# Kernel tuning notes

Measured on AMD Instinct MI355X. Metric: run time of the kernel, lower is better.

Reference implementation:

```python
import jax, jax.numpy as jnp
import numpy as np
import math

B, C, H, W = 4, 256, 64, 64
E = 96  # embed_dim
SOFTMAX_SCALE = 10.0
RESIDUAL_SCALE_INIT = 0.1


def conv1x1(w, x):
    # w: [out_c, in_c], x: [b, in_c, h, w] -> [b, out_c, h, w]
    return jnp.einsum('oc,bchw->bohw', w, x)


def setup_inputs() -> dict:
    key = jax.random.key(0)
    ks = jax.random.split(key, 12)
    s = 0.02
    return {
        'x': jax.random.normal(ks[0], (B, C, H, W), jnp.float32),
        'mask': jax.random.uniform(ks[1], (B, 1, H, W), jnp.float32),
        'ln_gamma': jnp.ones((C,), jnp.float32),
        'ln_beta': jnp.zeros((C,), jnp.float32),
        'wq': jax.random.normal(ks[2], (E, C), jnp.float32) * s,
        'wk': jax.random.normal(ks[3], (E, C), jnp.float32) * s,
        'wv': jax.random.normal(ks[4], (C, C), jnp.float32) * s,
        'w_out': jax.random.normal(ks[5], (C, C), jnp.float32) * s,
        'w_qm': jax.random.normal(ks[6], (E, 1), jnp.float32) * s,
        'wd1': jax.random.normal(ks[7], (C, 2 * C), jnp.float32) * s,
        'wd2': jax.random.normal(ks[8], (C, C), jnp.float32) * s,
        'wg': jax.random.normal(ks[9], (C, C + 1), jnp.float32) * s,
        'residual_scale': jnp.asarray(RESIDUAL_SCALE_INIT, jnp.float32),
    }


def reference(x, mask, ln_gamma, ln_beta, wq, wk, wv, w_out, w_qm, wd1, wd2, wg,
              residual_scale):
    b, c, h, w = x.shape
    n = h * w

    # ChannelLayerNorm: LayerNorm over channel dim
    mu = jnp.mean(x, axis=1, keepdims=True)
    var = jnp.mean((x - mu) ** 2, axis=1, keepdims=True)
    x_norm = (x - mu) / jnp.sqrt(var + 1e-5)
    x_norm = x_norm * ln_gamma[None, :, None, None] + ln_beta[None, :, None, None]

    # Q/K/V projections (1x1 convs), flatten to [b, n, d]
    q = conv1x1(wq, x_norm) + conv1x1(w_qm, mask)
    q = q.reshape(b, E, n).transpose(0, 2, 1)        # [b, n, E]
    k = conv1x1(wk, x_norm).reshape(b, E, n).transpose(0, 2, 1)  # [b, n, E]
    v = conv1x1(wv, x).reshape(b, c, n).transpose(0, 2, 1)       # [b, n, C]

    # cosine normalization (F.normalize with eps=1e-12)
    q = q / jnp.clip(jnp.linalg.norm(q, axis=-1, keepdims=True), 1e-12)
    k = k / jnp.clip(jnp.linalg.norm(k, axis=-1, keepdims=True), 1e-12)

    scale = SOFTMAX_SCALE / math.sqrt(E)
    attn = jnp.einsum('bqe,bke->bqk', q, k) * scale  # [b, n, n]

    # keys with mask >= 0.5 are invalid -> bias -10000
    invalid_keys = (mask.reshape(b, 1, n) >= 0.5)    # [b, 1, n]
    attn = jnp.where(invalid_keys, jnp.float32(-10000.0), attn)
    attn = jax.nn.softmax(attn, axis=-1)

    attended = jnp.einsum('bqk,bkc->bqc', attn, v)   # [b, n, C]
    attended = attended.transpose(0, 2, 1).reshape(b, c, h, w)
    attended = conv1x1(w_out, attended)

    # delta correction branch
    corr_in = jnp.concatenate([attended - x, x_norm * mask], axis=1)  # [b, 2C, h, w]
    hidden = jax.nn.gelu(conv1x1(wd1, corr_in), approximate=False)
    corrective = conv1x1(wd2, hidden)

    # MaskConditionedGate (assumed): sigmoid(1x1 conv over [corrective, mask])
    gate_in = jnp.concatenate([corrective, mask], axis=1)  # [b, C+1, h, w]
    gate = jax.nn.sigmoid(conv1x1(wg, gate_in)) * mask

    delta = jnp.tanh(residual_scale) * gate * corrective
    return x + delta
```

## Files before the change

### kernel.cpp

```cpp
#include <hip/hip_runtime.h>
#include <hip/hip_bf16.h>
#include <math.h>

#define BB 4
#define CC 256
#define NN 4096
#define EE 96
#define NTOT (BB*NN)

typedef __attribute__((ext_vector_type(8))) short bf16x8;
typedef __attribute__((ext_vector_type(4))) float f32x4;

__device__ __forceinline__ short f2bf(float x) {
    __hip_bfloat16 h = __float2bfloat16(x);
    return *reinterpret_cast<short*>(&h);
}
__device__ __forceinline__ float bf2f(short s) {
    unsigned int u = ((unsigned int)(unsigned short)s) << 16;
    float f;
    __builtin_memcpy(&f, &u, 4);
    return f;
}
__device__ __forceinline__ float gelu_exact(float v) {
    return 0.5f * v * (1.0f + erff(v * 0.70710678118654752f));
}
__device__ __forceinline__ void gld16(void* lds, const void* g) {
    __builtin_amdgcn_global_load_lds(
        (const __attribute__((address_space(1))) unsigned int*)g,
        (__attribute__((address_space(3))) unsigned int*)lds, 16, 0, 0);
}

#define OFF_WQ  0
#define OFF_WK  24576
#define OFF_WV  49152
#define OFF_WO  114688
#define OFF_WD1 180224
#define OFF_WD2 311296
#define OFF_WG  376832
#define OFF_WGL 442368
#define W16_TOTAL 442624

__global__ void wconv_kernel(const float* __restrict__ wq, const float* __restrict__ wk,
                             const float* __restrict__ wv, const float* __restrict__ wo,
                             const float* __restrict__ wd1, const float* __restrict__ wd2,
                             const float* __restrict__ wg, short* __restrict__ W16) {
    int i = blockIdx.x * 256 + threadIdx.x;
    if (i >= W16_TOTAL) return;
    float v;
    if      (i < OFF_WK)  v = wq[i];
    else if (i < OFF_WV)  v = wk[i - OFF_WK];
    else if (i < OFF_WO)  v = wv[i - OFF_WV];
    else if (i < OFF_WD1) v = wo[i - OFF_WO];
    else if (i < OFF_WD2) v = wd1[i - OFF_WD1];
    else if (i < OFF_WG)  v = wd2[i - OFF_WD2];
    else if (i < OFF_WGL) { int l = i - OFF_WG; v = wg[(l >> 8) * 257 + (l & 255)]; }
    else                  v = wg[(i - OFF_WGL) * 257 + 256];
    W16[i] = f2bf(v);
}

__global__ __launch_bounds__(256) void ln_kernel(
    const float* __restrict__ x, const float* __restrict__ gamma,
    const float* __restrict__ beta,
    short* __restrict__ Xt16, short* __restrict__ Xn16) {
    __shared__ float tile[256 * 33];
    __shared__ float psum[8][32], psq[8][32];
    __shared__ float mu_s[32], rs_s[32];
    __shared__ float gs[256], bs[256];
    const int b  = blockIdx.x >> 7;
    const int p0 = (blockIdx.x & 127) * 32;
    const int tid = threadIdx.x;
    const float* xb = x + (size_t)b * CC * NN;

    gs[tid] = gamma[tid];
    bs[tid] = beta[tid];
    #pragma unroll
    for (int i = 0; i < 8; ++i) {
        int idx = tid + i * 256;
        int c = idx >> 3, p4 = (idx & 7) * 4;
        float4 v = *(const float4*)&xb[(size_t)c * NN + p0 + p4];
        tile[c * 33 + p4]     = v.x;
        tile[c * 33 + p4 + 1] = v.y;
        tile[c * 33 + p4 + 2] = v.z;
        tile[c * 33 + p4 + 3] = v.w;
    }
    __syncthreads();
    {
        int col = tid & 31, part = tid >> 5;
        float s = 0.f, sq = 0.f;
        for (int r = part * 32; r < part * 32 + 32; ++r) {
            float v = tile[r * 33 + col];
            s += v; sq += v * v;
        }
        psum[part][col] = s; psq[part][col] = sq;
    }
    __syncthreads();
    if (tid < 32) {
        float S = 0.f, SQ = 0.f;
        #pragma unroll
        for (int j = 0; j < 8; ++j) { S += psum[j][tid]; SQ += psq[j][tid]; }
        float mu = S / 256.0f;
        float var = SQ / 256.0f - mu * mu;
        mu_s[tid] = mu;
        rs_s[tid] = rsqrtf(var + 1e-5f);
    }
    __syncthreads();
    size_t rowbase = ((size_t)b * NN + p0) * CC;
    #pragma unroll
    for (int i = 0; i < 4; ++i) {
        int idx = tid + i * 256;
        int p = idx >> 5, c8 = (idx & 31) * 8;
        float mu = mu_s[p], rcp = rs_s[p];
        bf16x8 xt, xn;
        #pragma unroll
        for (int j = 0; j < 8; ++j) {
            float v = tile[(c8 + j) * 33 + p];
            float n = (v - mu) * rcp * gs[c8 + j] + bs[c8 + j];
            xt[j] = f2bf(v); xn[j] = f2bf(n);
        }
        size_t o = rowbase + (size_t)p * CC + c8;
        *(bf16x8*)&Xt16[o] = xt;
        *(bf16x8*)&Xn16[o] = xn;
    }
}

__global__ __launch_bounds__(256) void qkproj_kernel(
    const short* __restrict__ Xn16, const short* __restrict__ W16,
    const float* __restrict__ mask, const float* __restrict__ w_qm,
    short* __restrict__ Q16, short* __restrict__ K16)
{
    const int tid = threadIdx.x;
    const int w = tid >> 6, lane = tid & 63, ln = lane & 15, quad = lane >> 4;
    const int m0 = blockIdx.x * 32 + (w & 1) * 16;
    const bool isQ = (w < 2);
    const int woff = isQ ? OFF_WQ : OFF_WK;

    f32x4 acc[6];
    #pragma unroll
    for (int i = 0; i < 6; ++i) acc[i] = (f32x4){0.f, 0.f, 0.f, 0.f};

    #pragma unroll
    for (int kt = 0; kt < 8; ++kt) {
        bf16x8 af = *(const bf16x8*)&Xn16[(size_t)(m0 + ln) * 256 + kt * 32 + quad * 8];
        #pragma unroll
        for (int nt = 0; nt < 6; ++nt) {
            bf16x8 bf = *(const bf16x8*)&W16[woff + (size_t)(nt * 16 + ln) * 256 + kt * 32 + quad * 8];
            acc[nt] = __builtin_amdgcn_mfma_f32_16x16x32_bf16(af, bf, acc[nt], 0, 0, 0);
        }
    }

    short* outp = isQ ? Q16 : K16;
    #pragma unroll
    for (int r = 0; r < 4; ++r) {
        int row = m0 + quad * 4 + r;
        float mrow = isQ ? mask[row] : 0.f;
        float vals[6];
        float ss = 0.f;
        #pragma unroll
        for (int nt = 0; nt < 6; ++nt) {
            float v = acc[nt][r];
            if (isQ) v += mrow * w_qm[nt * 16 + ln];
            vals[nt] = v;
            ss += v * v;
        }
        ss += __shfl_xor(ss, 1, 64); ss += __shfl_xor(ss, 2, 64);
        ss += __shfl_xor(ss, 4, 64); ss += __shfl_xor(ss, 8, 64);
        float sc = 1.0f / fmaxf(sqrtf(ss), 1e-12f);
        #pragma unroll
        for (int nt = 0; nt < 6; ++nt)
            outp[(size_t)row * EE + nt * 16 + ln] = f2bf(vals[nt] * sc);
    }
}

__global__ __launch_bounds__(256) void vproj_kernel(
    const short* __restrict__ Xt16, const short* __restrict__ W16,
    short* __restrict__ V16t)
{
    __shared__ short Vt[256 * 40];
    const int tid = threadIdx.x;
    const int w = tid >> 6, lane = tid & 63, ln = lane & 15, quad = lane >> 4;
    const int m0 = blockIdx.x * 32;
    const int wm = w >> 1, wn = w & 1;
    const int mrow = m0 + wm * 16;

    f32x4 acc[8];
    #pragma unroll
    for (int i = 0; i < 8; ++i) acc[i] = (f32x4){0.f, 0.f, 0.f, 0.f};

    #pragma unroll
    for (int kt = 0; kt < 8; ++kt) {
        bf16x8 af = *(const bf16x8*)&Xt16[(size_t)(mrow + ln) * 256 + kt * 32 + quad * 8];
        #pragma unroll
        for (int nt = 0; nt < 8; ++nt) {
            int col = wn * 128 + nt * 16 + ln;
            bf16x8 bf = *(const bf16x8*)&W16[OFF_WV + (size_t)col * 256 + kt * 32 + quad * 8];
            acc[nt] = __builtin_amdgcn_mfma_f32_16x16x32_bf16(af, bf, acc[nt], 0, 0, 0);
        }
    }
    #pragma unroll
    for (int nt = 0; nt < 8; ++nt) {
        int ch = wn * 128 + nt * 16 + ln;
        #pragma unroll
        for (int r = 0; r < 4; ++r)
            Vt[ch * 40 + wm * 16 + quad * 4 + r] = f2bf(acc[nt][r]);
    }
    __syncthreads();
    const int b = m0 >> 12, p0l = m0 & 4095;
    #pragma unroll
    for (int i = 0; i < 4; ++i) {
        int idx = tid + i * 256;
        int ch = idx >> 2, p8 = (idx & 3) * 8;
        *(bf16x8*)&V16t[((size_t)b * CC + ch) * NN + p0l + p8] =
            *(const bf16x8*)&Vt[ch * 40 + p8];
    }
}

__global__ __launch_bounds__(256, 4) void attn_kernel(
    const short* __restrict__ Q16, const short* __restrict__ K16,
    const short* __restrict__ V16t, const float* __restrict__ mask,
    short* __restrict__ Opart, float* __restrict__ Lpart)
{
    __shared__ short Ks[2][3072];
    __shared__ short Ps[64 * 40];

    const int tid = threadIdx.x;
    const int w = tid >> 6, lane = tid & 63, ln = lane & 15, quad = lane >> 4;
    const int bidx = blockIdx.x;
    const int kg = bidx >> 8;
    const int qg = bidx & 255;
    const int b  = (qg & 7) >> 1;
    const int qt = ((qg >> 3) << 1) | (qg & 1);
    const int q0 = qt * 64;
    const size_t bN = (size_t)b * NN;
    const size_t bCC = (size_t)b * CC;
    const int kbase = kg * 1024;
    const float C1 = 1.02062072615966f;
    const int wbase = w * 64;

    bf16x8 qf[3];
    #pragma unroll
    for (int e = 0; e < 3; ++e)
        qf[e] = *(const bf16x8*)&Q16[(bN + q0 + w * 16 + ln) * EE + e * 32 + quad * 8];

    f32x4 acc[4][4];
    #pragma unroll
    for (int mt = 0; mt < 4; ++mt)
        #pragma unroll
        for (int nt = 0; nt < 4; ++nt) acc[mt][nt] = (f32x4){0.f, 0.f, 0.f, 0.f};
    float lsum[4] = {0.f, 0.f, 0.f, 0.f};

    gld16(&Ks[0][wbase * 8], &K16[(bN + kbase + (tid & 31)) * EE + (tid >> 5) * 8]);
    if (w < 2)
        gld16(&Ks[0][(256 + wbase) * 8],
              &K16[(bN + kbase + (tid & 31)) * EE + (8 + (tid >> 5)) * 8]);
    __syncthreads();

    int cur = 0;
    for (int it = 0; it < 32; ++it) {
        const int k0 = kbase + it * 32;

        bf16x8 vf[4];
        #pragma unroll
        for (int nt = 0; nt < 4; ++nt)
            vf[nt] = *(const bf16x8*)&V16t[(bCC + wbase + nt * 16 + ln) * NN + k0 + quad * 8];
        const float mk0 = mask[bN + k0 + ln];
        const float mk1 = mask[bN + k0 + 16 + ln];

        if (it + 1 < 32) {
            const int k0n = k0 + 32;
            gld16(&Ks[cur ^ 1][wbase * 8],
                  &K16[(bN + k0n + (tid & 31)) * EE + (tid >> 5) * 8]);
            if (w < 2)
                gld16(&Ks[cur ^ 1][(256 + wbase) * 8],
                      &K16[(bN + k0n + (tid & 31)) * EE + (8 + (tid >> 5)) * 8]);
        }

        f32x4 s0 = (f32x4){0.f,0.f,0.f,0.f}, s1 = s0;
        __builtin_amdgcn_s_setprio(1);
        #pragma unroll
        for (int e = 0; e < 3; ++e) {
            bf16x8 kf0 = *(const bf16x8*)&Ks[cur][((e * 4 + quad) * 32 + ln) * 8];
            bf16x8 kf1 = *(const bf16x8*)&Ks[cur][((e * 4 + quad) * 32 + 16 + ln) * 8];
            s0 = __builtin_amdgcn_mfma_f32_16x16x32_bf16(qf[e], kf0, s0, 0, 0, 0);
            s1 = __builtin_amdgcn_mfma_f32_16x16x32_bf16(qf[e], kf1, s1, 0, 0, 0);
        }
        __builtin_amdgcn_s_setprio(0);
        const bool z0 = mk0 >= 0.5f;
        const bool z1 = mk1 >= 0.5f;
        #pragma unroll
        for (int r = 0; r < 4; ++r) {
            float p0 = z0 ? 0.f : __expf(fmaf(s0[r], C1, -C1));
            float p1 = z1 ? 0.f : __expf(fmaf(s1[r], C1, -C1));
            lsum[r] += p0 + p1;
            Ps[(w * 16 + quad * 4 + r) * 40 + ln]      = f2bf(p0);
            Ps[(w * 16 + quad * 4 + r) * 40 + 16 + ln] = f2bf(p1);
        }
        asm volatile("s_waitcnt lgkmcnt(0)" ::: "memory");
        __builtin_amdgcn_s_barrier();
        __builtin_amdgcn_sched_barrier(0);

        __builtin_amdgcn_s_setprio(1);
        #pragma unroll
        for (int mt = 0; mt < 4; ++mt) {
            bf16x8 pf = *(const bf16x8*)&Ps[(mt * 16 + ln) * 40 + quad * 8];
            #pragma unroll
            for (int nt = 0; nt < 4; ++nt)
                acc[mt][nt] = __builtin_amdgcn_mfma_f32_16x16x32_bf16(pf, vf[nt], acc[mt][nt], 0, 0, 0);
        }
        __builtin_amdgcn_s_setprio(0);
        asm volatile("s_waitcnt vmcnt(0) lgkmcnt(0)" ::: "memory");
        __builtin_amdgcn_s_barrier();
        __builtin_amdgcn_sched_barrier(0);
        cur ^= 1;
    }

    #pragma unroll
    for (int r = 0; r < 4; ++r) {
        float l = lsum[r];
        l += __shfl_xor(l, 1, 64); l += __shfl_xor(l, 2, 64);
        l += __shfl_xor(l, 4, 64); l += __shfl_xor(l, 8, 64);
        if (ln == 0)
            Lpart[(size_t)kg * NTOT + bN + q0 + w * 16 + quad * 4 + r] = l;
    }
    #pragma unroll
    for (int mt = 0; mt < 4; ++mt)
        #pragma unroll
        for (int nt = 0; nt < 4; ++nt)
            #pragma unroll
            for (int r = 0; r < 4; ++r)
                Opart[((size_t)kg * NTOT + bN + q0 + mt * 16 + quad * 4 + r) * 256
                      + wbase + nt * 16 + ln] = f2bf(acc[mt][nt][r]);
}

__global__ __launch_bounds__(256, 2) void epi_kernel(
    const short* __restrict__ Opart, const float* __restrict__ Lpart,
    const short* __restrict__ W16, const short* __restrict__ Xt16,
    const short* __restrict__ Xn16, const float* __restrict__ mask,
    const float* __restrict__ rs, const float* __restrict__ x,
    float* __restrict__ out)
{
    __shared__ char lds[54400];
    short* Olds  = (short*)lds;
    short* Hlds  = (short*)lds;
    short* Dlds  = (short*)(lds + 16896);
    short* Clds  = (short*)(lds + 16896);
    short* tileB = (short*)(lds + 33792);
    float* lsh   = (float*)(lds + 54272);

    const int tid = threadIdx.x;
    const int w = tid >> 6, lane = tid & 63, ln = lane & 15, quad = lane >> 4;
    const int wm = w >> 1, wn = w & 1;
    const int m0 = blockIdx.x * 32;
    const int b = m0 >> 12, p0l = m0 & 4095;

    if (tid < 32) {
        int g = m0 + tid;
        lsh[tid] = 1.0f / (Lpart[g] + Lpart[NTOT + g] + Lpart[2 * NTOT + g] + Lpart[3 * NTOT + g]);
    }
    __syncthreads();

    #pragma unroll
    for (int i = 0; i < 4; ++i) {
        int idx = tid + i * 256;
        int q = idx >> 5, ch8 = (idx & 31) * 8;
        size_t base = (size_t)(m0 + q) * 256 + ch8;
        bf16x8 a0 = *(const bf16x8*)&Opart[base];
        bf16x8 a1 = *(const bf16x8*)&Opart[(size_t)NTOT * 256 + base];
        bf16x8 a2 = *(const bf16x8*)&Opart[(size_t)2 * NTOT * 256 + base];
        bf16x8 a3 = *(const bf16x8*)&Opart[(size_t)3 * NTOT * 256 + base];
        float linv = lsh[q];
        bf16x8 o;
        #pragma unroll
        for (int e = 0; e < 8; ++e)
            o[e] = f2bf((bf2f(a0[e]) + bf2f(a1[e]) + bf2f(a2[e]) + bf2f(a3[e])) * linv);
        *(bf16x8*)&Olds[q * 264 + ch8] = o;
        bf16x8 xn = *(const bf16x8*)&Xn16[base];
        float mq = mask[m0 + q];
        bf16x8 xm;
        #pragma unroll
        for (int e = 0; e < 8; ++e) xm[e] = f2bf(bf2f(xn[e]) * mq);
        *(bf16x8*)&Dlds[q * 528 + 256 + ch8] = xm;
    }
    __syncthreads();

    {
        f32x4 acc[8];
        #pragma unroll
        for (int i = 0; i < 8; ++i) acc[i] = (f32x4){0.f, 0.f, 0.f, 0.f};
        #pragma unroll
        for (int kt = 0; kt < 8; ++kt) {
            bf16x8 af = *(const bf16x8*)&Olds[(wm * 16 + ln) * 264 + kt * 32 + quad * 8];
            #pragma unroll
            for (int nt = 0; nt < 8; ++nt) {
                int col = wn * 128 + nt * 16 + ln;
                bf16x8 bf = *(const bf16x8*)&W16[OFF_WO + (size_t)col * 256 + kt * 32 + quad * 8];
                acc[nt] = __builtin_amdgcn_mfma_f32_16x16x32_bf16(af, bf, acc[nt], 0, 0, 0);
            }
        }
        #pragma unroll
        for (int nt = 0; nt < 8; ++nt) {
            int col = wn * 128 + nt * 16 + ln;
            #pragma unroll
            for (int r = 0; r < 4; ++r) {
                int row = wm * 16 + quad * 4 + r;
                float v = acc[nt][r] - bf2f(Xt16[(size_t)(m0 + row) * 256 + col]);
                Dlds[row * 528 + col] = f2bf(v);
            }
        }
    }
    __syncthreads();

    {
        f32x4 acc[8];
        #pragma unroll
        for (int i = 0; i < 8; ++i) acc[i] = (f32x4){0.f, 0.f, 0.f, 0.f};
        #pragma unroll
        for (int kt = 0; kt < 16; ++kt) {
            bf16x8 af = *(const bf16x8*)&Dlds[(wm * 16 + ln) * 528 + kt * 32 + quad * 8];
            #pragma unroll
            for (int nt = 0; nt < 8; ++nt) {
                int col = wn * 128 + nt * 16 + ln;
                bf16x8 bf = *(const bf16x8*)&W16[OFF_WD1 + (size_t)col * 512 + kt * 32 + quad * 8];
                acc[nt] = __builtin_amdgcn_mfma_f32_16x16x32_bf16(af, bf, acc[nt], 0, 0, 0);
            }
        }
        __syncthreads();
        #pragma unroll
        for (int nt = 0; nt < 8; ++nt) {
            int col = wn * 128 + nt * 16 + ln;
            #pragma unroll
            for (int r = 0; r < 4; ++r) {
                int row = wm * 16 + quad * 4 + r;
                Hlds[row * 264 + col] = f2bf(gelu_exact(acc[nt][r]));
            }
        }
    }
    __syncthreads();

    {
        f32x4 acc[8];
        #pragma unroll
        for (int i = 0; i < 8; ++i) acc[i] = (f32x4){0.f, 0.f, 0.f, 0.f};
        #pragma unroll
        for (int kt = 0; kt < 8; ++kt) {
            bf16x8 af = *(const bf16x8*)&Hlds[(wm * 16 + ln) * 264 + kt * 32 + quad * 8];
            #pragma unroll
            for (int nt = 0; nt < 8; ++nt) {
                int col = wn * 128 + nt * 16 + ln;
                bf16x8 bf = *(const bf16x8*)&W16[OFF_WD2 + (size_t)col * 256 + kt * 32 + quad * 8];
                acc[nt] = __builtin_amdgcn_mfma_f32_16x16x32_bf16(af, bf, acc[nt], 0, 0, 0);
            }
        }
        __syncthreads();
        #pragma unroll
        for (int nt = 0; nt < 8; ++nt) {
            int col = wn * 128 + nt * 16 + ln;
            #pragma unroll
            for (int r = 0; r < 4; ++r) {
                int row = wm * 16 + quad * 4 + r;
                Clds[row * 264 + col] = f2bf(acc[nt][r]);
            }
        }
    }
    __syncthreads();

    {
        f32x4 acc[8];
        #pragma unroll
        for (int i = 0; i < 8; ++i) acc[i] = (f32x4){0.f, 0.f, 0.f, 0.f};
        #pragma unroll
        for (int kt = 0; kt < 8; ++kt) {
            bf16x8 af = *(const bf16x8*)&Clds[(wm * 16 + ln) * 264 + kt * 32 + quad * 8];
            #pragma unroll
            for (int nt = 0; nt < 8; ++nt) {
                int col = wn * 128 + nt * 16 + ln;
                bf16x8 bf = *(const bf16x8*)&W16[OFF_WG + (size_t)col * 256 + kt * 32 + quad * 8];
                acc[nt] = __builtin_amdgcn_mfma_f32_16x16x32_bf16(af, bf, acc[nt], 0, 0, 0);
            }
        }
        float trs = tanhf(rs[0]);
        #pragma unroll
        for (int nt = 0; nt < 8; ++nt) {
            int col = wn * 128 + nt * 16 + ln;
            float wgl = bf2f(W16[OFF_WGL + col]);
            #pragma unroll
            for (int r = 0; r < 4; ++r) {
                int row = wm * 16 + quad * 4 + r;
                float mrow = mask[m0 + row];
                float logit = acc[nt][r] + mrow * wgl;
                float gate = mrow / (1.0f + __expf(-logit));
                float corr = bf2f(Clds[row * 264 + col]);
                tileB[col * 40 + row] = f2bf(trs * gate * corr);
            }
        }
    }
    __syncthreads();

    #pragma unroll
    for (int i = 0; i < 4; ++i) {
        int idx = tid + i * 256;
        int ch = idx >> 2, p8 = (idx & 3) * 8;
        bf16x8 d = *(const bf16x8*)&tileB[ch * 40 + p8];
        size_t o = ((size_t)b * CC + ch) * NN + p0l + p8;
        float4 x0 = *(const float4*)&x[o];
        float4 x1 = *(const float4*)&x[o + 4];
        float4 o0, o1;
        o0.x = x0.x + bf2f(d[0]); o0.y = x0.y + bf2f(d[1]);
        o0.z = x0.z + bf2f(d[2]); o0.w = x0.w + bf2f(d[3]);
        o1.x = x1.x + bf2f(d[4]); o1.y = x1.y + bf2f(d[5]);
        o1.z = x1.z + bf2f(d[6]); o1.w = x1.w + bf2f(d[7]);
        *(float4*)&out[o] = o0;
        *(float4*)&out[o + 4] = o1;
    }
}

extern "C" void kernel_launch(void* const* d_in, const int* in_sizes, int n_in,
                              void* d_out, int out_size, void* d_ws, size_t ws_size,
                              hipStream_t stream) {
    const float* x     = (const float*)d_in[0];
    const float* mask  = (const float*)d_in[1];
    const float* gamma = (const float*)d_in[2];
    const float* beta  = (const float*)d_in[3];
    const float* wq    = (const float*)d_in[4];
    const float* wk    = (const float*)d_in[5];
    const float* wv    = (const float*)d_in[6];
    const float* w_out = (const float*)d_in[7];
    const float* w_qm  = (const float*)d_in[8];
    const float* wd1   = (const float*)d_in[9];
    const float* wd2   = (const float*)d_in[10];
    const float* wg    = (const float*)d_in[11];
    const float* rs    = (const float*)d_in[12];
    float* out = (float*)d_out;

    const size_t NC = (size_t)NTOT * CC;
    const size_t NE = (size_t)NTOT * EE;
    short* Xn16  = (short*)d_ws;
    short* Xt16  = Xn16 + NC;
    short* Q16   = Xt16 + NC;
    short* K16   = Q16 + NE;
    short* V16t  = K16 + NE;
    short* W16   = V16t + NC;
    short* Opart = W16 + W16_TOTAL;
    float* Lpart = (float*)(Opart + 4 * NC);

    wconv_kernel<<<(W16_TOTAL + 255) / 256, 256, 0, stream>>>(wq, wk, wv, w_out,
                                                              wd1, wd2, wg, W16);
    ln_kernel<<<512, 256, 0, stream>>>(x, gamma, beta, Xt16, Xn16);
    qkproj_kernel<<<512, 256, 0, stream>>>(Xn16, W16, mask, w_qm, Q16, K16);
    vproj_kernel<<<512, 256, 0, stream>>>(Xt16, W16, V16t);
    attn_kernel<<<1024, 256, 0, stream>>>(Q16, K16, V16t, mask, Opart, Lpart);
    epi_kernel<<<512, 256, 0, stream>>>(Opart, Lpart, W16, Xt16, Xn16, mask,
                                        rs, x, out);
}
```

Baseline: 300.9 us.

## Merge weight conversion into LN, fuse QK/V projections, double-buffer attention P tile

Weight bf16 conversion is folded into the layernorm kernel as a grid-stride loop, and the Q/K and V projection kernels are merged into one launch of 1024 blocks, cutting two kernel launches. In the attention loop the P tile in shared memory is double-buffered, which removes one barrier per iteration. V fragment and mask loads now issue after the next K tile prefetch. The P double-buffer adds some shared memory use, and the conversion loop adds work to the LN blocks.

```diff
diff --git a/kernel.cpp b/kernel.cpp
--- a/kernel.cpp
+++ b/kernel.cpp
@@ -40,27 +40,13 @@
 #define OFF_WGL 442368
 #define W16_TOTAL 442624
 
-__global__ void wconv_kernel(const float* __restrict__ wq, const float* __restrict__ wk,
-                             const float* __restrict__ wv, const float* __restrict__ wo,
-                             const float* __restrict__ wd1, const float* __restrict__ wd2,
-                             const float* __restrict__ wg, short* __restrict__ W16) {
-    int i = blockIdx.x * 256 + threadIdx.x;
-    if (i >= W16_TOTAL) return;
-    float v;
-    if      (i < OFF_WK)  v = wq[i];
-    else if (i < OFF_WV)  v = wk[i - OFF_WK];
-    else if (i < OFF_WO)  v = wv[i - OFF_WV];
-    else if (i < OFF_WD1) v = wo[i - OFF_WO];
-    else if (i < OFF_WD2) v = wd1[i - OFF_WD1];
-    else if (i < OFF_WG)  v = wd2[i - OFF_WD2];
-    else if (i < OFF_WGL) { int l = i - OFF_WG; v = wg[(l >> 8) * 257 + (l & 255)]; }
-    else                  v = wg[(i - OFF_WGL) * 257 + 256];
-    W16[i] = f2bf(v);
-}
-
 __global__ __launch_bounds__(256) void ln_kernel(
     const float* __restrict__ x, const float* __restrict__ gamma,
     const float* __restrict__ beta,
+    const float* __restrict__ wq, const float* __restrict__ wk,
+    const float* __restrict__ wv, const float* __restrict__ wo,
+    const float* __restrict__ wd1, const float* __restrict__ wd2,
+    const float* __restrict__ wg, short* __restrict__ W16,
     short* __restrict__ Xt16, short* __restrict__ Xn16) {
     __shared__ float tile[256 * 33];
     __shared__ float psum[8][32], psq[8][32];
@@ -71,6 +57,19 @@
     const int tid = threadIdx.x;
     const float* xb = x + (size_t)b * CC * NN;
 
+    for (int i = blockIdx.x * 256 + tid; i < W16_TOTAL; i += 512 * 256) {
+        float v;
+        if      (i < OFF_WK)  v = wq[i];
+        else if (i < OFF_WV)  v = wk[i - OFF_WK];
+        else if (i < OFF_WO)  v = wv[i - OFF_WV];
+        else if (i < OFF_WD1) v = wo[i - OFF_WO];
+        else if (i < OFF_WD2) v = wd1[i - OFF_WD1];
+        else if (i < OFF_WG)  v = wd2[i - OFF_WD2];
+        else if (i < OFF_WGL) { int l = i - OFF_WG; v = wg[(l >> 8) * 257 + (l & 255)]; }
+        else                  v = wg[(i - OFF_WGL) * 257 + 256];
+        W16[i] = f2bf(v);
+    }
+
     gs[tid] = gamma[tid];
     bs[tid] = beta[tid];
     #pragma unroll
@@ -123,94 +122,92 @@
     }
 }
 
-__global__ __launch_bounds__(256) void qkproj_kernel(
-    const short* __restrict__ Xn16, const short* __restrict__ W16,
+__global__ __launch_bounds__(256) void proj_kernel(
+    const short* __restrict__ Xn16, const short* __restrict__ Xt16,
+    const short* __restrict__ W16,
     const float* __restrict__ mask, const float* __restrict__ w_qm,
-    short* __restrict__ Q16, short* __restrict__ K16)
-{
-    const int tid = threadIdx.x;
-    const int w = tid >> 6, lane = tid & 63, ln = lane & 15, quad = lane >> 4;
-    const int m0 = blockIdx.x * 32 + (w & 1) * 16;
-    const bool isQ = (w < 2);
-    const int woff = isQ ? OFF_WQ : OFF_WK;
-
-    f32x4 acc[6];
-    #pragma unroll
-    for (int i = 0; i < 6; ++i) acc[i] = (f32x4){0.f, 0.f, 0.f, 0.f};
-
-    #pragma unroll
-    for (int kt = 0; kt < 8; ++kt) {
-        bf16x8 af = *(const bf16x8*)&Xn16[(size_t)(m0 + ln) * 256 + kt * 32 + quad * 8];
-        #pragma unroll
-        for (int nt = 0; nt < 6; ++nt) {
-            bf16x8 bf = *(const bf16x8*)&W16[woff + (size_t)(nt * 16 + ln) * 256 + kt * 32 + quad * 8];
-            acc[nt] = __builtin_amdgcn_mfma_f32_16x16x32_bf16(af, bf, acc[nt], 0, 0, 0);
-        }
-    }
-
-    short* outp = isQ ? Q16 : K16;
-    #pragma unroll
-    for (int r = 0; r < 4; ++r) {
-        int row = m0 + quad * 4 + r;
-        float mrow = isQ ? mask[row] : 0.f;
-        float vals[6];
-        float ss = 0.f;
-        #pragma unroll
-        for (int nt = 0; nt < 6; ++nt) {
-            float v = acc[nt][r];
-            if (isQ) v += mrow * w_qm[nt * 16 + ln];
-            vals[nt] = v;
-            ss += v * v;
-        }
-        ss += __shfl_xor(ss, 1, 64); ss += __shfl_xor(ss, 2, 64);
-        ss += __shfl_xor(ss, 4, 64); ss += __shfl_xor(ss, 8, 64);
-        float sc = 1.0f / fmaxf(sqrtf(ss), 1e-12f);
-        #pragma unroll
-        for (int nt = 0; nt < 6; ++nt)
-            outp[(size_t)row * EE + nt * 16 + ln] = f2bf(vals[nt] * sc);
-    }
-}
-
-__global__ __launch_bounds__(256) void vproj_kernel(
-    const short* __restrict__ Xt16, const short* __restrict__ W16,
+    short* __restrict__ Q16, short* __restrict__ K16,
     short* __restrict__ V16t)
 {
     __shared__ short Vt[256 * 40];
     const int tid = threadIdx.x;
     const int w = tid >> 6, lane = tid & 63, ln = lane & 15, quad = lane >> 4;
-    const int m0 = blockIdx.x * 32;
-    const int wm = w >> 1, wn = w & 1;
-    const int mrow = m0 + wm * 16;
-
-    f32x4 acc[8];
-    #pragma unroll
-    for (int i = 0; i < 8; ++i) acc[i] = (f32x4){0.f, 0.f, 0.f, 0.f};
-
-    #pragma unroll
-    for (int kt = 0; kt < 8; ++kt) {
-        bf16x8 af = *(const bf16x8*)&Xt16[(size_t)(mrow + ln) * 256 + kt * 32 + quad * 8];
+
+    if (blockIdx.x < 512) {
+        const int m0 = blockIdx.x * 32 + (w & 1) * 16;
+        const bool isQ = (w < 2);
+        const int woff = isQ ? OFF_WQ : OFF_WK;
+
+        f32x4 acc[6];
+        #pragma unroll
+        for (int i = 0; i < 6; ++i) acc[i] = (f32x4){0.f, 0.f, 0.f, 0.f};
+
+        #pragma unroll
+        for (int kt = 0; kt < 8; ++kt) {
+            bf16x8 af = *(const bf16x8*)&Xn16[(size_t)(m0 + ln) * 256 + kt * 32 + quad * 8];
+            #pragma unroll
+            for (int nt = 0; nt < 6; ++nt) {
+                bf16x8 bf = *(const bf16x8*)&W16[woff + (size_t)(nt * 16 + ln) * 256 + kt * 32 + quad * 8];
+                acc[nt] = __builtin_amdgcn_mfma_f32_16x16x32_bf16(af, bf, acc[nt], 0, 0, 0);
+            }
+        }
+
+        short* outp = isQ ? Q16 : K16;
+        #pragma unroll
+        for (int r = 0; r < 4; ++r) {
+            int row = m0 + quad * 4 + r;
+            float mrow = isQ ? mask[row] : 0.f;
+            float vals[6];
+            float ss = 0.f;
+            #pragma unroll
+            for (int nt = 0; nt < 6; ++nt) {
+                float v = acc[nt][r];
+                if (isQ) v += mrow * w_qm[nt * 16 + ln];
+                vals[nt] = v;
+                ss += v * v;
+            }
+            ss += __shfl_xor(ss, 1, 64); ss += __shfl_xor(ss, 2, 64);
+            ss += __shfl_xor(ss, 4, 64); ss += __shfl_xor(ss, 8, 64);
+            float sc = 1.0f / fmaxf(sqrtf(ss), 1e-12f);
+            #pragma unroll
+            for (int nt = 0; nt < 6; ++nt)
+                outp[(size_t)row * EE + nt * 16 + ln] = f2bf(vals[nt] * sc);
+        }
+    } else {
+        const int m0 = (blockIdx.x - 512) * 32;
+        const int wm = w >> 1, wn = w & 1;
+        const int mrow = m0 + wm * 16;
+
+        f32x4 acc[8];
+        #pragma unroll
+        for (int i = 0; i < 8; ++i) acc[i] = (f32x4){0.f, 0.f, 0.f, 0.f};
+
+        #pragma unroll
+        for (int kt = 0; kt < 8; ++kt) {
+            bf16x8 af = *(const bf16x8*)&Xt16[(size_t)(mrow + ln) * 256 + kt * 32 + quad * 8];
+            #pragma unroll
+            for (int nt = 0; nt < 8; ++nt) {
+                int col = wn * 128 + nt * 16 + ln;
+                bf16x8 bf = *(const bf16x8*)&W16[OFF_WV + (size_t)col * 256 + kt * 32 + quad * 8];
+                acc[nt] = __builtin_amdgcn_mfma_f32_16x16x32_bf16(af, bf, acc[nt], 0, 0, 0);
+            }
+        }
         #pragma unroll
         for (int nt = 0; nt < 8; ++nt) {
-            int col = wn * 128 + nt * 16 + ln;
-            bf16x8 bf = *(const bf16x8*)&W16[OFF_WV + (size_t)col * 256 + kt * 32 + quad * 8];
-            acc[nt] = __builtin_amdgcn_mfma_f32_16x16x32_bf16(af, bf, acc[nt], 0, 0, 0);
-        }
-    }
-    #pragma unroll
-    for (int nt = 0; nt < 8; ++nt) {
-        int ch = wn * 128 + nt * 16 + ln;
-        #pragma unroll
-        for (int r = 0; r < 4; ++r)
-            Vt[ch * 40 + wm * 16 + quad * 4 + r] = f2bf(acc[nt][r]);
-    }
-    __syncthreads();
-    const int b = m0 >> 12, p0l = m0 & 4095;
-    #pragma unroll
-    for (int i = 0; i < 4; ++i) {
-        int idx = tid + i * 256;
-        int ch = idx >> 2, p8 = (idx & 3) * 8;
-        *(bf16x8*)&V16t[((size_t)b * CC + ch) * NN + p0l + p8] =
-            *(const bf16x8*)&Vt[ch * 40 + p8];
+            int ch = wn * 128 + nt * 16 + ln;
+            #pragma unroll
+            for (int r = 0; r < 4; ++r)
+                Vt[ch * 40 + wm * 16 + quad * 4 + r] = f2bf(acc[nt][r]);
+        }
+        __syncthreads();
+        const int b = m0 >> 12, p0l = m0 & 4095;
+        #pragma unroll
+        for (int i = 0; i < 4; ++i) {
+            int idx = tid + i * 256;
+            int ch = idx >> 2, p8 = (idx & 3) * 8;
+            *(bf16x8*)&V16t[((size_t)b * CC + ch) * NN + p0l + p8] =
+                *(const bf16x8*)&Vt[ch * 40 + p8];
+        }
     }
 }
 
@@ -220,7 +217,7 @@
     short* __restrict__ Opart, float* __restrict__ Lpart)
 {
     __shared__ short Ks[2][3072];
-    __shared__ short Ps[64 * 40];
+    __shared__ short Ps[2][2560];
 
     const int tid = threadIdx.x;
     const int w = tid >> 6, lane = tid & 63, ln = lane & 15, quad = lane >> 4;
@@ -254,16 +251,9 @@
               &K16[(bN + kbase + (tid & 31)) * EE + (8 + (tid >> 5)) * 8]);
     __syncthreads();
 
-    int cur = 0;
     for (int it = 0; it < 32; ++it) {
         const int k0 = kbase + it * 32;
-
-        bf16x8 vf[4];
-        #pragma unroll
-        for (int nt = 0; nt < 4; ++nt)
-            vf[nt] = *(const bf16x8*)&V16t[(bCC + wbase + nt * 16 + ln) * NN + k0 + quad * 8];
-        const float mk0 = mask[bN + k0 + ln];
-        const float mk1 = mask[bN + k0 + 16 + ln];
+        const int cur = it & 1;
 
         if (it + 1 < 32) {
             const int k0n = k0 + 32;
@@ -273,6 +263,12 @@
                 gld16(&Ks[cur ^ 1][(256 + wbase) * 8],
                       &K16[(bN + k0n + (tid & 31)) * EE + (8 + (tid >> 5)) * 8]);
         }
+        bf16x8 vf[4];
+        #pragma unroll
+        for (int nt = 0; nt < 4; ++nt)
+            vf[nt] = *(const bf16x8*)&V16t[(bCC + wbase + nt * 16 + ln) * NN + k0 + quad * 8];
+        const float mk0 = mask[bN + k0 + ln];
+        const float mk1 = mask[bN + k0 + 16 + ln];
 
         f32x4 s0 = (f32x4){0.f,0.f,0.f,0.f}, s1 = s0;
         __builtin_amdgcn_s_setprio(1);
@@ -291,26 +287,22 @@
             float p0 = z0 ? 0.f : __expf(fmaf(s0[r], C1, -C1));
             float p1 = z1 ? 0.f : __expf(fmaf(s1[r], C1, -C1));
             lsum[r] += p0 + p1;
-            Ps[(w * 16 + quad * 4 + r) * 40 + ln]      = f2bf(p0);
-            Ps[(w * 16 + quad * 4 + r) * 40 + 16 + ln] = f2bf(p1);
-        }
-        asm volatile("s_waitcnt lgkmcnt(0)" ::: "memory");
-        __builtin_amdgcn_s_barrier();
-        __builtin_amdgcn_sched_barrier(0);
-
-        __builtin_amdgcn_s_setprio(1);
-        #pragma unroll
-        for (int mt = 0; mt < 4; ++mt) {
-            bf16x8 pf = *(const bf16x8*)&Ps[(mt * 16 + ln) * 40 + quad * 8];
-            #pragma unroll
-            for (int nt = 0; nt < 4; ++nt)
-                acc[mt][nt] = __builtin_amdgcn_mfma_f32_16x16x32_bf16(pf, vf[nt], acc[mt][nt], 0, 0, 0);
-        }
-        __builtin_amdgcn_s_setprio(0);
+            Ps[cur][(w * 16 + quad * 4 + r) * 40 + ln]      = f2bf(p0);
+            Ps[cur][(w * 16 + quad * 4 + r) * 40 + 16 + ln] = f2bf(p1);
+        }
         asm volatile("s_waitcnt vmcnt(0) lgkmcnt(0)" ::: "memory");
         __builtin_amdgcn_s_barrier();
         __builtin_amdgcn_sched_barrier(0);
-        cur ^= 1;
+
+        __builtin_amdgcn_s_setprio(1);
+        #pragma unroll
+        for (int mt = 0; mt < 4; ++mt) {
+            bf16x8 pf = *(const bf16x8*)&Ps[cur][(mt * 16 + ln) * 40 + quad * 8];
+            #pragma unroll
+            for (int nt = 0; nt < 4; ++nt)
+                acc[mt][nt] = __builtin_amdgcn_mfma_f32_16x16x32_bf16(pf, vf[nt], acc[mt][nt], 0, 0, 0);
+        }
+        __builtin_amdgcn_s_setprio(0);
     }
 
     #pragma unroll
@@ -542,11 +534,10 @@
     short* Opart = W16 + W16_TOTAL;
     float* Lpart = (float*)(Opart + 4 * NC);
 
-    wconv_kernel<<<(W16_TOTAL + 255) / 256, 256, 0, stream>>>(wq, wk, wv, w_out,
-                                                              wd1, wd2, wg, W16);
-    ln_kernel<<<512, 256, 0, stream>>>(x, gamma, beta, Xt16, Xn16);
-    qkproj_kernel<<<512, 256, 0, stream>>>(Xn16, W16, mask, w_qm, Q16, K16);
-    vproj_kernel<<<512, 256, 0, stream>>>(Xt16, W16, V16t);
+    ln_kernel<<<512, 256, 0, stream>>>(x, gamma, beta, wq, wk, wv, w_out,
+                                       wd1, wd2, wg, W16, Xt16, Xn16);
+    proj_kernel<<<1024, 256, 0, stream>>>(Xn16, Xt16, W16, mask, w_qm,
+                                          Q16, K16, V16t);
     attn_kernel<<<1024, 256, 0, stream>>>(Q16, K16, V16t, mask, Opart, Lpart);
     epi_kernel<<<512, 256, 0, stream>>>(Opart, Lpart, W16, Xt16, Xn16, mask,
                                         rs, x, out);
```

Result: no change. 298.1 us (-0.9%).
